# Performance work log

Measured on AMD Instinct MI355X. Metric: run time of the kernel, lower is better.

The kernel has to match this reference:

```python
import jax, jax.numpy as jnp
from jax import lax
import numpy as np

HEADS = 8

def _hswish(x):
    return x * jnp.clip(x + 3.0, 0.0, 6.0) / 6.0

def _sep_conv(x, dw, pw, pad):
    # depthwise conv (groups=C) followed by 1x1 pointwise conv, no bias
    dn = ('NCHW', 'OIHW', 'NCHW')
    y = lax.conv_general_dilated(x, dw, (1, 1), [(pad, pad), (pad, pad)],
                                 dimension_numbers=dn, feature_group_count=x.shape[1])
    return lax.conv_general_dilated(y, pw, (1, 1), [(0, 0), (0, 0)], dimension_numbers=dn)

def _bn(x, g, b, m, v):
    # SyncBatchNorm in eval mode (running stats), eps=1e-5
    inv = g / jnp.sqrt(v + 1e-5)
    return (x - m[:, None, None]) * inv[:, None, None] + b[:, None, None]

def _gn(x, g, b, groups=2):
    B, C, H, W = x.shape
    xg = x.reshape(B, groups, -1)
    mu = xg.mean(-1, keepdims=True)
    var = xg.var(-1, keepdims=True)
    xg = (xg - mu) / jnp.sqrt(var + 1e-5)
    return xg.reshape(B, C, H, W) * g[:, None, None] + b[:, None, None]

def _ln(x, g, b):
    mu = x.mean(-1, keepdims=True)
    var = x.var(-1, keepdims=True)
    return (x - mu) / jnp.sqrt(var + 1e-5) * g + b

def _forward(fl, h, w):
    (x, ln_q_g, ln_q_b, ln_k_g, ln_k_b, ln_v_g, ln_v_b, w_q, w_k, w_v, w_proj, b_proj,
     dw0, pw0, gn_g, gn_b, dw1, pw1, dw2, pw2,
     bn0_g, bn0_b, bn0_m, bn0_v, bn1_g, bn1_b, bn1_m, bn1_v, bn2_g, bn2_b, bn2_m, bn2_v) = fl
    B, C, N = x.shape  # C = attr_num tokens, N = dim = h*w
    d = N // HEADS
    scale = d ** -0.5
    q = _ln(x, ln_q_g, ln_q_b) @ w_q.T
    k = _ln(x, ln_k_g, ln_k_b) @ w_k.T
    v = _ln(x, ln_v_g, ln_v_b) @ w_v.T

    def agg(t):
        # aggregator(t.transpose(1,2), (h,w)) then head split; net input is (B,C,h,w)
        img = t.reshape(B, C, h, w)
        p0, p1, p2, p3 = jnp.split(img, 4, axis=1)  # seg_dim = C//4
        x0 = _hswish(_bn(p0, bn0_g, bn0_b, bn0_m, bn0_v))
        x1 = _hswish(_bn(_sep_conv(p1, dw1, pw1, 1), bn1_g, bn1_b, bn1_m, bn1_v))
        x2 = _hswish(_bn(_sep_conv(p2, dw2, pw2, 2), bn2_g, bn2_b, bn2_m, bn2_v))
        xl = _hswish(_gn(_sep_conv(p3, dw0, pw0, 1), gn_g, gn_b))
        y = jnp.concatenate([x0, x1, x2, xl], axis=1).reshape(B, C, N)
        return y.reshape(B, C, HEADS, d).transpose(0, 2, 1, 3)  # (B,H,C,d)

    qh, kh, vh = agg(q), agg(k), agg(v)
    scores = jnp.einsum('bhcd,bhkd->bhck', qh, kh)
    attn = jax.nn.softmax(jax.nn.gelu(scores, approximate=False) * scale, axis=-1)
    out = jnp.einsum('bhck,bhkd->bhcd', attn, vh).reshape(B, C, N)  # raw reshape as in torch
    out = out @ w_proj.T + b_proj
    out = out / jnp.maximum(jnp.linalg.norm(out, axis=-1, keepdims=True), 1e-12)
    return out, attn


def setup_inputs() -> dict:
    key = jax.random.key(0)
    ks = jax.random.split(key, 12)
    B, C, N = 32, 312, 1024
    sd = C // 4  # 78
    f32 = jnp.float32
    rn = lambda k, shp, s: jax.random.normal(k, shp, f32) * s
    inp = {
        'x': rn(ks[0], (B, C, N), 1.0),
        'h': 32, 'w': 32,
        'ln_q_g': jnp.ones((N,), f32), 'ln_q_b': jnp.zeros((N,), f32),
        'ln_k_g': jnp.ones((N,), f32), 'ln_k_b': jnp.zeros((N,), f32),
        'ln_v_g': jnp.ones((N,), f32), 'ln_v_b': jnp.zeros((N,), f32),
        'w_q': rn(ks[1], (N, N), N ** -0.5),
        'w_k': rn(ks[2], (N, N), N ** -0.5),
        'w_v': rn(ks[3], (N, N), N ** -0.5),
        'w_proj': rn(ks[4], (N, N), N ** -0.5),
        'b_proj': jnp.zeros((N,), f32),
        'dw0': rn(ks[5], (sd, 1, 3, 3), 1.0 / 3.0),
        'pw0': rn(ks[6], (sd, sd, 1, 1), sd ** -0.5),
        'gn_g': jnp.ones((sd,), f32), 'gn_b': jnp.zeros((sd,), f32),
        'dw1': rn(ks[7], (sd, 1, 3, 3), 1.0 / 3.0),
        'pw1': rn(ks[8], (sd, sd, 1, 1), sd ** -0.5),
        'dw2': rn(ks[9], (sd, 1, 5, 5), 1.0 / 5.0),
        'pw2': rn(ks[10], (sd, sd, 1, 1), sd ** -0.5),
    }
    for i in range(3):
        inp[f'bn{i}_g'] = jnp.ones((sd,), f32)
        inp[f'bn{i}_b'] = jnp.zeros((sd,), f32)
        inp[f'bn{i}_m'] = jnp.zeros((sd,), f32)
        inp[f'bn{i}_v'] = jnp.ones((sd,), f32)
    return inp


def reference(x, h, w, ln_q_g, ln_q_b, ln_k_g, ln_k_b, ln_v_g, ln_v_b, w_q, w_k, w_v, w_proj, b_proj, dw0, pw0, gn_g, gn_b, dw1, pw1, dw2, pw2, bn0_g, bn0_b, bn0_m, bn0_v, bn1_g, bn1_b, bn1_m, bn1_v, bn2_g, bn2_b, bn2_m, bn2_v):
    fl = (x, ln_q_g, ln_q_b, ln_k_g, ln_k_b, ln_v_g, ln_v_b, w_q, w_k, w_v, w_proj, b_proj,
          dw0, pw0, gn_g, gn_b, dw1, pw1, dw2, pw2,
          bn0_g, bn0_b, bn0_m, bn0_v, bn1_g, bn1_b, bn1_m, bn1_v, bn2_g, bn2_b, bn2_m, bn2_v)
    return _forward(fl, h, w)
```

## Files before the change

### kernel.cpp

```cpp
#include <hip/hip_runtime.h>
#include <hip/hip_bf16.h>
#include <float.h>

typedef __hip_bfloat16 bf16;
typedef __attribute__((ext_vector_type(8))) __bf16 bfrag;
typedef __attribute__((ext_vector_type(4))) float f32x4;

#define B_ 32
#define C_ 312
#define N_ 1024
#define H_ 8
#define D_ 128
#define SD_ 78
#define BC_ (B_ * C_)
#define BH_ (B_ * H_)

__device__ __forceinline__ float bf2f(bf16 x) { return __bfloat162float(x); }
__device__ __forceinline__ bf16 f2bf(float x) { return __float2bfloat16(x); }
__device__ __forceinline__ float hswish(float x) {
    return x * fminf(fmaxf(x + 3.0f, 0.0f), 6.0f) * (1.0f / 6.0f);
}

__device__ __forceinline__ void gload_lds16(const void* g, void* l) {
    __builtin_amdgcn_global_load_lds(
        (const __attribute__((address_space(1))) void*)g,
        (__attribute__((address_space(3))) void*)l, 16, 0, 0);
}

__global__ void ln_kernel(const float* __restrict__ x, bf16* __restrict__ xn) {
    int r = blockIdx.x;
    int t = threadIdx.x;
    const float* xr = x + (size_t)r * N_;
    float4 v4 = *reinterpret_cast<const float4*>(xr + t * 4);
    float s = v4.x + v4.y + v4.z + v4.w;
    float sq = v4.x * v4.x + v4.y * v4.y + v4.z * v4.z + v4.w * v4.w;
    __shared__ float rs[256], rq[256];
    rs[t] = s; rq[t] = sq; __syncthreads();
    for (int o = 128; o > 0; o >>= 1) {
        if (t < o) { rs[t] += rs[t + o]; rq[t] += rq[t + o]; }
        __syncthreads();
    }
    float mu = rs[0] * (1.0f / N_);
    float var = rq[0] * (1.0f / N_) - mu * mu;
    float rstd = rsqrtf(var + 1e-5f);
    __bf16 o4[4] = { (__bf16)((v4.x - mu) * rstd), (__bf16)((v4.y - mu) * rstd),
                     (__bf16)((v4.z - mu) * rstd), (__bf16)((v4.w - mu) * rstd) };
    *reinterpret_cast<uint2*>(reinterpret_cast<__bf16*>(xn) + (size_t)r * N_ + t * 4) =
        *reinterpret_cast<const uint2*>(o4);
}

__global__ void wcvt_kernel(const float* __restrict__ wq, const float* __restrict__ wk,
                            const float* __restrict__ wv, const float* __restrict__ wp,
                            const float* __restrict__ gq, const float* __restrict__ bq,
                            const float* __restrict__ gk, const float* __restrict__ bk,
                            const float* __restrict__ gv, const float* __restrict__ bv_,
                            bf16* __restrict__ wqkv, float* __restrict__ bias3,
                            bf16* __restrict__ wpb) {
    int n = blockIdx.x;
    int t = threadIdx.x;
    int k4 = t * 4;
    const float* src; const float* G = nullptr; const float* Bv = nullptr;
    if (n < 1024)      { src = wq + (size_t)n * N_;          G = gq; Bv = bq; }
    else if (n < 2048) { src = wk + (size_t)(n - 1024) * N_; G = gk; Bv = bk; }
    else if (n < 3072) { src = wv + (size_t)(n - 2048) * N_; G = gv; Bv = bv_; }
    else               { src = wp + (size_t)(n - 3072) * N_; }
    float4 w4 = *reinterpret_cast<const float4*>(src + k4);
    if (G) {
        __bf16 o[4] = { (__bf16)(w4.x * G[k4]),     (__bf16)(w4.y * G[k4 + 1]),
                        (__bf16)(w4.z * G[k4 + 2]), (__bf16)(w4.w * G[k4 + 3]) };
        *reinterpret_cast<uint2*>(wqkv + (size_t)n * N_ + k4) = *reinterpret_cast<const uint2*>(o);
        float s = w4.x * Bv[k4] + w4.y * Bv[k4 + 1] + w4.z * Bv[k4 + 2] + w4.w * Bv[k4 + 3];
        __shared__ float rs[256];
        rs[t] = s; __syncthreads();
        for (int o2 = 128; o2 > 0; o2 >>= 1) {
            if (t < o2) rs[t] += rs[t + o2];
            __syncthreads();
        }
        if (t == 0) bias3[n] = rs[0];
    } else {
        __bf16 o[4] = { (__bf16)w4.x, (__bf16)w4.y, (__bf16)w4.z, (__bf16)w4.w };
        *reinterpret_cast<uint2*>(wpb + (size_t)(n - 3072) * N_ + k4) = *reinterpret_cast<const uint2*>(o);
    }
}

template <bool OUTF32>
__global__ __launch_bounds__(256) void mfma_gemm_bw(
        const bf16* __restrict__ A_,
        const bf16* __restrict__ Wb,
        const float* __restrict__ bias, int nTx,
        void* __restrict__ O0, void* __restrict__ O1, void* __restrict__ O2) {
    const int K = 1024, Nout = 1024;
    __shared__ __bf16 sA[128 * 64];
    __shared__ __bf16 sB[128 * 64];
    const __bf16* A = reinterpret_cast<const __bf16*>(A_);
    const __bf16* W = reinterpret_cast<const __bf16*>(Wb);

    int t = threadIdx.x;
    int lane = t & 63, wave = t >> 6;
    int wm = (wave >> 1) * 64, wn = (wave & 1) * 64;
    int quad = lane >> 4, l15 = lane & 15;

    int cpx = gridDim.x >> 3;
    int tile = (blockIdx.x & 7) * cpx + (blockIdx.x >> 3);
    int bx = tile % nTx, by = tile / nTx;
    int m0 = by * 128;
    int w0 = bx * 128;
    int which = bx >> 3;
    int n0 = (bx & 7) * 128;

    int rowLoc = wave * 8 + (lane >> 3);
    int c8s = (lane & 7) ^ (lane >> 3);
    const __bf16* gA = A + (size_t)(m0 + rowLoc) * K + c8s * 8;
    const __bf16* gW = W + (size_t)(w0 + rowLoc) * K + c8s * 8;

    f32x4 acc[4][4];
#pragma unroll
    for (int i = 0; i < 4; i++)
#pragma unroll
        for (int j = 0; j < 4; j++) acc[i][j] = (f32x4)(0.f);

    for (int kt = 0; kt < 16; kt++) {
        int k0 = kt * 64;
#pragma unroll
        for (int cc = 0; cc < 4; cc++) {
            gload_lds16(gA + (size_t)cc * 32 * K + k0, &sA[cc * 2048 + wave * 512]);
            gload_lds16(gW + (size_t)cc * 32 * K + k0, &sB[cc * 2048 + wave * 512]);
        }
        __syncthreads();
#pragma unroll
        for (int kk = 0; kk < 2; kk++) {
            bfrag af[4], bfr[4];
#pragma unroll
            for (int mt = 0; mt < 4; mt++) {
                int row = wm + mt * 16 + l15;
                af[mt] = *reinterpret_cast<const bfrag*>(
                    &sA[(row * 8 + ((kk * 4 + quad) ^ (row & 7))) * 8]);
            }
#pragma unroll
            for (int nt = 0; nt < 4; nt++) {
                int row = wn + nt * 16 + l15;
                bfr[nt] = *reinterpret_cast<const bfrag*>(
                    &sB[(row * 8 + ((kk * 4 + quad) ^ (row & 7))) * 8]);
            }
#pragma unroll
            for (int mt = 0; mt < 4; mt++)
#pragma unroll
                for (int nt = 0; nt < 4; nt++)
                    acc[mt][nt] = __builtin_amdgcn_mfma_f32_16x16x32_bf16(af[mt], bfr[nt], acc[mt][nt], 0, 0, 0);
        }
        __syncthreads();
    }
    void* Cout = which == 0 ? O0 : (which == 1 ? O1 : O2);
#pragma unroll
    for (int mt = 0; mt < 4; mt++) {
#pragma unroll
        for (int nt = 0; nt < 4; nt++) {
            int cloc = wn + nt * 16 + l15;
            float bb = bias ? bias[w0 + cloc] : 0.f;
            int col = n0 + cloc;
#pragma unroll
            for (int r = 0; r < 4; r++) {
                int row = m0 + wm + mt * 16 + quad * 4 + r;
                float v = acc[mt][nt][r] + bb;
                if (OUTF32) ((float*)Cout)[(size_t)row * Nout + col] = v;
                else        ((bf16*)Cout)[(size_t)row * Nout + col] = f2bf(v);
            }
        }
    }
}

__global__ void seg0_kernel(const bf16* __restrict__ t0, const bf16* __restrict__ t1,
                            const bf16* __restrict__ t2,
                            bf16* __restrict__ h0, bf16* __restrict__ h1,
                            bf16* __restrict__ h2,
                            const float* __restrict__ g, const float* __restrict__ b,
                            const float* __restrict__ m, const float* __restrict__ v) {
    int ti = blockIdx.y;
    const bf16* tin = ti == 0 ? t0 : (ti == 1 ? t1 : t2);
    bf16* th = ti == 0 ? h0 : (ti == 1 ? h1 : h2);
    int bc = blockIdx.x;
    int bi = bc / SD_, c = bc % SD_;
    float inv = g[c] * rsqrtf(v[c] + 1e-5f);
    float mm = m[c], bb = b[c];
    const __bf16* tp = reinterpret_cast<const __bf16*>(tin) + ((size_t)bi * C_ + c) * N_;
    __bf16* base = reinterpret_cast<__bf16*>(th) + (size_t)bi * H_ * C_ * D_;
    int n = threadIdx.x * 4;
    uint2 in2 = *reinterpret_cast<const uint2*>(tp + n);
    const __bf16* iv = reinterpret_cast<const __bf16*>(&in2);
    __bf16 o4[4];
#pragma unroll
    for (int j = 0; j < 4; j++)
        o4[j] = (__bf16)hswish(((float)iv[j] - mm) * inv + bb);
    *reinterpret_cast<uint2*>(&base[((n >> 7) * C_ + c) * D_ + (n & 127)]) =
        *reinterpret_cast<const uint2*>(o4);
}

template <int KS, int MODE>
__device__ __forceinline__ void dwpw_impl(
        char* uMem, float* sWk, __bf16* dwT,
        const bf16* __restrict__ tin, int cOff,
        const float* __restrict__ dw, const float* __restrict__ pw,
        const float* __restrict__ g, const float* __restrict__ b,
        const float* __restrict__ m, const float* __restrict__ v,
        bf16* __restrict__ th, float* __restrict__ rawOut,
        int strip, int bi, int tid) {
    constexpr int WKP = ((KS * KS + 3) / 4) * 4;
    constexpr int NR  = KS + 1;
    __bf16* sIn = reinterpret_cast<__bf16*>(uMem);
    __bf16* sWm = reinterpret_cast<__bf16*>(uMem);
    const int P = KS / 2;

    for (int u = tid; u < SD_ * NR * 2; u += 512) {
        int rowi = u >> 1, side = u & 1;
        *reinterpret_cast<uint2*>(sIn + rowi * 40 + (side ? 36 : 0)) = make_uint2(0u, 0u);
    }
    for (int u = tid; u < 64 * 9; u += 512) {
        int pos = u / 9, cc = 78 + (u % 9) * 2;
        *reinterpret_cast<unsigned int*>(dwT + pos * 96 + cc) = 0u;
    }
    const __bf16* tbase = reinterpret_cast<const __bf16*>(tin) + ((size_t)bi * C_ + cOff) * N_;
    for (int u = tid; u < SD_ * NR * 4; u += 512) {
        int c = u / (NR * 4);
        int rem = u - c * (NR * 4);
        int di = rem >> 2, cb = rem & 3;
        int ii = 2 * strip + di - P;
        uint4 val = make_uint4(0u, 0u, 0u, 0u);
        if (ii >= 0 && ii <= 31)
            val = *reinterpret_cast<const uint4*>(tbase + (size_t)c * N_ + ii * 32 + cb * 8);
        __bf16* dst = sIn + (c * NR + di) * 40 + 4 + cb * 8;
        *reinterpret_cast<uint2*>(dst)     = make_uint2(val.x, val.y);
        *reinterpret_cast<uint2*>(dst + 4) = make_uint2(val.z, val.w);
    }
    for (int i = tid; i < SD_ * KS * KS; i += 512) {
        int c = i / (KS * KS), q = i - c * (KS * KS);
        sWk[c * WKP + q] = dw[i];
    }
    __syncthreads();

    for (int u = tid; u < SD_ * 8; u += 512) {
        int c = u >> 3, grp = u & 7;
        int row = grp >> 2, q8 = (grp & 3) << 3;
        const __bf16* rbase = sIn + (size_t)(c * NR + row) * 40;
        __bf16 rowv[KS][16];
#pragma unroll
        for (int di = 0; di < KS; di++) {
            *reinterpret_cast<bfrag*>(&rowv[di][0]) = *reinterpret_cast<const bfrag*>(rbase + di * 40 + q8);
            *reinterpret_cast<bfrag*>(&rowv[di][8]) = *reinterpret_cast<const bfrag*>(rbase + di * 40 + q8 + 8);
        }
        float wreg[WKP];
#pragma unroll
        for (int qq = 0; qq < WKP / 4; qq++)
            *reinterpret_cast<float4*>(&wreg[qq * 4]) =
                *reinterpret_cast<const float4*>(&sWk[c * WKP + qq * 4]);
        float acc8[8];
#pragma unroll
        for (int k = 0; k < 8; k++) acc8[k] = 0.f;
#pragma unroll
        for (int di = 0; di < KS; di++) {
#pragma unroll
            for (int dj = 0; dj < KS; dj++) {
                float w = wreg[di * KS + dj];
#pragma unroll
                for (int k = 0; k < 8; k++)
                    acc8[k] += (float)rowv[di][k + dj - P + 4] * w;
            }
        }
#pragma unroll
        for (int k = 0; k < 8; k++)
            dwT[(row * 32 + q8 + k) * 96 + c] = (__bf16)acc8[k];
    }
    __syncthreads();

    for (int u = tid; u < 80 * 96; u += 512) {
        int o = u / 96, c = u - o * 96;
        float val = (o < SD_ && c < SD_) ? pw[o * SD_ + c] : 0.f;
        sWm[u] = (__bf16)val;
    }
    __syncthreads();

    int lane = tid & 63, wave = tid >> 6;
    int quad = lane >> 4, l15 = lane & 15;
    int wn = wave & 3, mh = wave >> 2;
    int mt0 = mh ? 3 : 0;
    int mcnt = mh ? 2 : 3;
    f32x4 acc[3];
#pragma unroll
    for (int i = 0; i < 3; i++) acc[i] = (f32x4)(0.f);
#pragma unroll
    for (int kk = 0; kk < 3; kk++) {
        bfrag bv = *reinterpret_cast<const bfrag*>(dwT + (wn * 16 + l15) * 96 + kk * 32 + quad * 8);
#pragma unroll
        for (int mi = 0; mi < 3; mi++) {
            if (mi < mcnt) {
                bfrag av = *reinterpret_cast<const bfrag*>(sWm + ((mt0 + mi) * 16 + l15) * 96 + kk * 32 + quad * 8);
                acc[mi] = __builtin_amdgcn_mfma_f32_16x16x32_bf16(av, bv, acc[mi], 0, 0, 0);
            }
        }
    }
    int n = strip * 64 + wn * 16 + l15;
    if (MODE == 0) {
        bf16* base = th + (size_t)bi * H_ * C_ * D_;
#pragma unroll
        for (int mi = 0; mi < 3; mi++) {
            if (mi < mcnt) {
#pragma unroll
                for (int r = 0; r < 4; r++) {
                    int o = (mt0 + mi) * 16 + quad * 4 + r;
                    if (o < SD_) {
                        float inv = g[o] * rsqrtf(v[o] + 1e-5f);
                        float y = hswish((acc[mi][r] - m[o]) * inv + b[o]);
                        base[((n >> 7) * C_ + cOff + o) * D_ + (n & 127)] = f2bf(y);
                    }
                }
            }
        }
    } else {
        float* opr = rawOut + (size_t)bi * SD_ * N_;
#pragma unroll
        for (int mi = 0; mi < 3; mi++) {
            if (mi < mcnt) {
#pragma unroll
                for (int r = 0; r < 4; r++) {
                    int o = (mt0 + mi) * 16 + quad * 4 + r;
                    if (o < SD_) opr[(size_t)o * N_ + n] = acc[mi][r];
                }
            }
        }
    }
}

__global__ __launch_bounds__(512) void dwpw_all_kernel(
        const bf16* __restrict__ t0, const bf16* __restrict__ t1,
        const bf16* __restrict__ t2,
        const float* __restrict__ dw1, const float* __restrict__ pw1,
        const float* __restrict__ g1, const float* __restrict__ b1,
        const float* __restrict__ m1, const float* __restrict__ v1,
        const float* __restrict__ dw2, const float* __restrict__ pw2,
        const float* __restrict__ g2, const float* __restrict__ b2,
        const float* __restrict__ m2, const float* __restrict__ v2,
        const float* __restrict__ dw0, const float* __restrict__ pw0,
        bf16* __restrict__ h0, bf16* __restrict__ h1, bf16* __restrict__ h2,
        float* __restrict__ r0_, float* __restrict__ r1_, float* __restrict__ r2_) {
    __shared__ __align__(16) char uMem[SD_ * 6 * 40 * sizeof(__bf16)];
    __shared__ __align__(16) float sWk[SD_ * 28];
    __shared__ __align__(16) __bf16 dwT[64 * 96];

    int ti = blockIdx.y;
    const bf16* tin = ti == 0 ? t0 : (ti == 1 ? t1 : t2);
    bf16* th = ti == 0 ? h0 : (ti == 1 ? h1 : h2);
    float* rawOut = ti == 0 ? r0_ : (ti == 1 ? r1_ : r2_);
    int strip = blockIdx.x & 15;
    int bi = blockIdx.x >> 4;
    int tid = threadIdx.x;
    int branch = blockIdx.z;

    if (branch == 0) {
        dwpw_impl<3, 0>(uMem, sWk, dwT, tin, SD_, dw1, pw1, g1, b1, m1, v1,
                        th, (float*)nullptr, strip, bi, tid);
    } else if (branch == 1) {
        dwpw_impl<5, 0>(uMem, sWk, dwT, tin, 2 * SD_, dw2, pw2, g2, b2, m2, v2,
                        th, (float*)nullptr, strip, bi, tid);
    } else {
        dwpw_impl<3, 1>(uMem, sWk, dwT, tin, 3 * SD_, dw0, pw0,
                        (const float*)nullptr, (const float*)nullptr,
                        (const float*)nullptr, (const float*)nullptr,
                        (bf16*)nullptr, rawOut, strip, bi, tid);
    }
}

__global__ void gn_stats_kernel(const float* __restrict__ r0_, const float* __restrict__ r1_,
                                const float* __restrict__ r2_, float* __restrict__ stats) {
    int ti = blockIdx.y;
    const float* tmp2 = ti == 0 ? r0_ : (ti == 1 ? r1_ : r2_);
    int bg = blockIdx.x;
    int bi = bg >> 1, grp = bg & 1;
    const float* p = tmp2 + (size_t)bi * SD_ * N_ + (size_t)grp * 39 * N_;
    float s = 0.f, sq = 0.f;
    const int TOT = 39 * N_;
    for (int i = threadIdx.x * 4; i < TOT; i += 1024) {
        float4 f4 = *reinterpret_cast<const float4*>(p + i);
        s += f4.x + f4.y + f4.z + f4.w;
        sq += f4.x * f4.x + f4.y * f4.y + f4.z * f4.z + f4.w * f4.w;
    }
    __shared__ float rs[256], rq[256];
    rs[threadIdx.x] = s; rq[threadIdx.x] = sq; __syncthreads();
    for (int o = 128; o > 0; o >>= 1) {
        if (threadIdx.x < o) { rs[threadIdx.x] += rs[threadIdx.x + o]; rq[threadIdx.x] += rq[threadIdx.x + o]; }
        __syncthreads();
    }
    if (threadIdx.x == 0) {
        float mu = rs[0] / (float)TOT;
        float var = rq[0] / (float)TOT - mu * mu;
        stats[ti * 128 + bg * 2] = mu;
        stats[ti * 128 + bg * 2 + 1] = rsqrtf(var + 1e-5f);
    }
}

__global__ void gn_apply_kernel(const float* __restrict__ r0_, const float* __restrict__ r1_,
                                const float* __restrict__ r2_, const float* __restrict__ stats,
                                const float* __restrict__ gg, const float* __restrict__ gb,
                                bf16* __restrict__ h0, bf16* __restrict__ h1,
                                bf16* __restrict__ h2) {
    int ti = blockIdx.y;
    const float* tmp2 = ti == 0 ? r0_ : (ti == 1 ? r1_ : r2_);
    bf16* th = ti == 0 ? h0 : (ti == 1 ? h1 : h2);
    int bc = blockIdx.x;
    int bi = bc / SD_, c = bc % SD_;
    int grp = c / 39;
    float mu = stats[ti * 128 + (bi * 2 + grp) * 2];
    float rstd = stats[ti * 128 + (bi * 2 + grp) * 2 + 1];
    float sc = gg[c] * rstd;
    float of = gb[c] - mu * sc;
    const float* p = tmp2 + ((size_t)bi * SD_ + c) * N_;
    __bf16* base = reinterpret_cast<__bf16*>(th) + (size_t)bi * H_ * C_ * D_;
    int n = threadIdx.x * 4;
    float4 f4 = *reinterpret_cast<const float4*>(p + n);
    __bf16 o4[4] = { (__bf16)hswish(f4.x * sc + of), (__bf16)hswish(f4.y * sc + of),
                     (__bf16)hswish(f4.z * sc + of), (__bf16)hswish(f4.w * sc + of) };
    *reinterpret_cast<uint2*>(&base[((n >> 7) * C_ + 234 + c) * D_ + (n & 127)]) =
        *reinterpret_cast<const uint2*>(o4);
}

#define SLDA 136
#define PLDA 328
__global__ __launch_bounds__(512, 4) void attn_av_kernel(
        const bf16* __restrict__ qh_, const bf16* __restrict__ kh_,
        const bf16* __restrict__ vh_,
        float* __restrict__ attnOut, bf16* __restrict__ ctx) {
    __shared__ __align__(16) char uni[60928];
    __shared__ float smax[64][2];
    __shared__ float ssum[64][2];
    __bf16* sQ = reinterpret_cast<__bf16*>(uni);
    __bf16* sK = reinterpret_cast<__bf16*>(uni + 17408);
    __bf16* sP = reinterpret_cast<__bf16*>(uni);
    __bf16* sV = reinterpret_cast<__bf16*>(uni + 41984);
    const __bf16* qh = reinterpret_cast<const __bf16*>(qh_);
    const __bf16* kh = reinterpret_cast<const __bf16*>(kh_);
    const __bf16* vh = reinterpret_cast<const __bf16*>(vh_);

    int strip = blockIdx.x;
    int bh = blockIdx.y;
    int t = threadIdx.x;
    int lane = t & 63, wave = t >> 6;
    int quad = lane >> 4, l15 = lane & 15;
    int wm = wave >> 1;
    int wn = wave & 1;

#pragma unroll
    for (int cc = 0; cc < 2; cc++) {
        int c = t + cc * 512;
        int row = c >> 4, seg = c & 15;
        int src = strip * 64 + row; if (src > 311) src = 311;
        bfrag v = *reinterpret_cast<const bfrag*>(qh + ((size_t)bh * C_ + src) * D_ + seg * 8);
        *reinterpret_cast<bfrag*>(&sQ[row * SLDA + seg * 8]) = v;
    }

    f32x4 acc[10];
#pragma unroll
    for (int i = 0; i < 10; i++) acc[i] = (f32x4)(0.f);

    bfrag af[4];
    bool afLoaded = false;

    for (int half = 0; half < 2; half++) {
        if (half) __syncthreads();
        for (int cc = 0; cc < 5; cc++) {
            int c = t + cc * 512;
            int row = c >> 4, seg = c & 15;
            int src = half * 160 + row;
            bfrag v;
            if (src < C_) {
                v = *reinterpret_cast<const bfrag*>(kh + ((size_t)bh * C_ + src) * D_ + seg * 8);
            } else {
#pragma unroll
                for (int j = 0; j < 8; j++) v[j] = (__bf16)0.f;
            }
            *reinterpret_cast<bfrag*>(&sK[row * SLDA + seg * 8]) = v;
        }
        __syncthreads();
        if (!afLoaded) {
#pragma unroll
            for (int ks = 0; ks < 4; ks++)
                af[ks] = *reinterpret_cast<const bfrag*>(&sQ[(wm * 16 + l15) * SLDA + ks * 32 + quad * 8]);
            afLoaded = true;
        }
#pragma unroll
        for (int ks = 0; ks < 4; ks++) {
#pragma unroll
            for (int jj = 0; jj < 5; jj++) {
                int lr = (wn * 5 + jj) * 16 + l15;
                bfrag bf = *reinterpret_cast<const bfrag*>(&sK[lr * SLDA + ks * 32 + quad * 8]);
                acc[half * 5 + jj] = __builtin_amdgcn_mfma_f32_16x16x32_bf16(af[ks], bf, acc[half * 5 + jj], 0, 0, 0);
            }
        }
    }

    const float scale = 0.08838834764831845f;
    const float inv_sqrt2 = 0.7071067811865475f;
#pragma unroll
    for (int a = 0; a < 10; a++) {
        int gt = (a / 5) * 10 + wn * 5 + (a % 5);
        int col = gt * 16 + l15;
#pragma unroll
        for (int r = 0; r < 4; r++) {
            float v = acc[a][r];
            float ge = 0.5f * v * (1.0f + erff(v * inv_sqrt2));
            float s = ge * scale;
            if (col >= C_) s = -FLT_MAX;
            acc[a][r] = s;
        }
    }
    float mx[4];
#pragma unroll
    for (int r = 0; r < 4; r++) {
        float m = -FLT_MAX;
#pragma unroll
        for (int a = 0; a < 10; a++) m = fmaxf(m, acc[a][r]);
        for (int o = 1; o < 16; o <<= 1) m = fmaxf(m, __shfl_xor(m, o));
        mx[r] = m;
    }
    if (l15 == 0) {
#pragma unroll
        for (int r = 0; r < 4; r++) smax[wm * 16 + quad * 4 + r][wn] = mx[r];
    }
    __syncthreads();
    float sm[4];
#pragma unroll
    for (int r = 0; r < 4; r++) {
        int row = wm * 16 + quad * 4 + r;
        float m = fmaxf(smax[row][0], smax[row][1]);
        float s = 0.f;
#pragma unroll
        for (int a = 0; a < 10; a++) {
            float e = __expf(acc[a][r] - m);
            acc[a][r] = e;
            s += e;
        }
        for (int o = 1; o < 16; o <<= 1) s += __shfl_xor(s, o);
        sm[r] = s;
    }
    if (l15 == 0) {
#pragma unroll
        for (int r = 0; r < 4; r++) ssum[wm * 16 + quad * 4 + r][wn] = sm[r];
    }
    __syncthreads();

#pragma unroll
    for (int r = 0; r < 4; r++) {
        int row = wm * 16 + quad * 4 + r;
        float inv = 1.0f / (ssum[row][0] + ssum[row][1]);
        int grow = strip * 64 + row;
        float* ao = attnOut + ((size_t)bh * C_ + grow) * C_;
#pragma unroll
        for (int a = 0; a < 10; a++) {
            int gt = (a / 5) * 10 + wn * 5 + (a % 5);
            int col = gt * 16 + l15;
            float pv = acc[a][r] * inv;
            if (grow < C_ && col < C_) ao[col] = pv;
            sP[row * PLDA + col] = f2bf(pv);
        }
    }

    f32x4 acc2[4];
#pragma unroll
    for (int i = 0; i < 4; i++) acc2[i] = (f32x4)(0.f);

    auto stageV = [&](int chunk) {
#pragma unroll
        for (int it = 0; it < 2; it++) {
            int g = t + it * 512;
            int d = g & 127;
            int oct = g >> 7;
            int ktl = oct >> 2, quad2 = oct & 3;
            int cb = chunk * 64 + ktl * 32 + quad2 * 8;
            const __bf16* vp = vh + ((size_t)bh * C_ + cb) * D_ + d;
            bfrag v;
            if (cb + 7 < C_) {
#pragma unroll
                for (int j = 0; j < 8; j++) v[j] = vp[(size_t)j * D_];
            } else {
#pragma unroll
                for (int j = 0; j < 8; j++) v[j] = (cb + j < C_) ? vp[(size_t)j * D_] : (__bf16)0.f;
            }
            *reinterpret_cast<bfrag*>(&sV[(((ktl * 8 + (d >> 4)) * 64) + quad2 * 16 + (d & 15)) * 8]) = v;
        }
    };

    stageV(0);
    __syncthreads();

    for (int chunk = 0; chunk < 5; chunk++) {
#pragma unroll
        for (int ktl = 0; ktl < 2; ktl++) {
            bfrag a = *reinterpret_cast<const bfrag*>(
                &sP[(wm * 16 + l15) * PLDA + chunk * 64 + ktl * 32 + quad * 8]);
#pragma unroll
            for (int ntl = 0; ntl < 4; ntl++) {
                int ntg = wn * 4 + ntl;
                bfrag b = *reinterpret_cast<const bfrag*>(&sV[(((ktl * 8 + ntg) * 64) + lane) * 8]);
                acc2[ntl] = __builtin_amdgcn_mfma_f32_16x16x32_bf16(a, b, acc2[ntl], 0, 0, 0);
            }
        }
        if (chunk < 4) {
            __syncthreads();
            stageV(chunk + 1);
            __syncthreads();
        }
    }

    int b = bh >> 3, h = bh & 7;
#pragma unroll
    for (int ntl = 0; ntl < 4; ntl++) {
        int d = wn * 64 + ntl * 16 + l15;
#pragma unroll
        for (int r = 0; r < 4; r++) {
            int c = strip * 64 + wm * 16 + quad * 4 + r;
            if (c < C_) {
                size_t oi = ((size_t)b * C_ + h * 39 + (c >> 3)) * N_ + ((c & 7) << 7) + d;
                ctx[oi] = f2bf(acc2[ntl][r]);
            }
        }
    }
}

__global__ void norm_kernel(const float* __restrict__ out3, float* __restrict__ outp) {
    int r = blockIdx.x;
    const float* p = out3 + (size_t)r * N_;
    float4 f4 = *reinterpret_cast<const float4*>(p + threadIdx.x * 4);
    float sq = f4.x * f4.x + f4.y * f4.y + f4.z * f4.z + f4.w * f4.w;
    __shared__ float rq[256];
    rq[threadIdx.x] = sq; __syncthreads();
    for (int o = 128; o > 0; o >>= 1) {
        if (threadIdx.x < o) rq[threadIdx.x] += rq[threadIdx.x + o];
        __syncthreads();
    }
    float inv = 1.0f / fmaxf(sqrtf(rq[0]), 1e-12f);
    float4 o4 = { f4.x * inv, f4.y * inv, f4.z * inv, f4.w * inv };
    *reinterpret_cast<float4*>(outp + (size_t)r * N_ + threadIdx.x * 4) = o4;
}

extern "C" void kernel_launch(void* const* d_in, const int* in_sizes, int n_in,
                              void* d_out, int out_size, void* d_ws, size_t ws_size,
                              hipStream_t stream) {
    const float* x      = (const float*)d_in[0];
    const float* ln_q_g = (const float*)d_in[3];
    const float* ln_q_b = (const float*)d_in[4];
    const float* ln_k_g = (const float*)d_in[5];
    const float* ln_k_b = (const float*)d_in[6];
    const float* ln_v_g = (const float*)d_in[7];
    const float* ln_v_b = (const float*)d_in[8];
    const float* w_q    = (const float*)d_in[9];
    const float* w_k    = (const float*)d_in[10];
    const float* w_v    = (const float*)d_in[11];
    const float* w_proj = (const float*)d_in[12];
    const float* b_proj = (const float*)d_in[13];
    const float* dw0    = (const float*)d_in[14];
    const float* pw0    = (const float*)d_in[15];
    const float* gn_g   = (const float*)d_in[16];
    const float* gn_b   = (const float*)d_in[17];
    const float* dw1    = (const float*)d_in[18];
    const float* pw1    = (const float*)d_in[19];
    const float* dw2    = (const float*)d_in[20];
    const float* pw2    = (const float*)d_in[21];
    const float* bn0_g  = (const float*)d_in[22];
    const float* bn0_b  = (const float*)d_in[23];
    const float* bn0_m  = (const float*)d_in[24];
    const float* bn0_v  = (const float*)d_in[25];
    const float* bn1_g  = (const float*)d_in[26];
    const float* bn1_b  = (const float*)d_in[27];
    const float* bn1_m  = (const float*)d_in[28];
    const float* bn1_v  = (const float*)d_in[29];
    const float* bn2_g  = (const float*)d_in[30];
    const float* bn2_b  = (const float*)d_in[31];
    const float* bn2_m  = (const float*)d_in[32];
    const float* bn2_v  = (const float*)d_in[33];

    char* ws = (char*)d_ws;
    size_t off = 0;
    auto alloc = [&](size_t bytes) {
        void* p = ws + off;
        off = (off + bytes + 255) & ~(size_t)255;
        return p;
    };
    const size_t BF_BYTES = (size_t)BC_ * N_ * sizeof(bf16);
    const size_t T2_FLOATS = (size_t)B_ * SD_ * N_;
    bf16*  xn   = (bf16*)alloc(BF_BYTES);
    bf16*  qb   = (bf16*)alloc(BF_BYTES);
    bf16*  kb   = (bf16*)alloc(BF_BYTES);
    bf16*  vb   = (bf16*)alloc(BF_BYTES);
    float* tmp2 = (float*)alloc(3 * T2_FLOATS * sizeof(float));
    float* gnst = (float*)alloc(2048);
    bf16*  wqkv = (bf16*)alloc((size_t)3 * N_ * N_ * sizeof(bf16));
    float* bias3 = (float*)alloc((size_t)3 * N_ * sizeof(float));
    bf16*  wpb  = (bf16*)alloc((size_t)N_ * N_ * sizeof(bf16));

    float* out_main = (float*)d_out;
    float* attn_out = out_main + (size_t)BC_ * N_;

    bf16* qh  = xn;
    bf16* kh  = (bf16*)out_main;
    bf16* vh  = kh + (size_t)BC_ * N_;
    bf16* ctx = vb;
    float* out3 = (float*)qb;
    float* r0 = tmp2, *r1 = tmp2 + T2_FLOATS, *r2 = tmp2 + 2 * T2_FLOATS;

    hipLaunchKernelGGL(wcvt_kernel, dim3(4096), dim3(256), 0, stream,
                       w_q, w_k, w_v, w_proj,
                       ln_q_g, ln_q_b, ln_k_g, ln_k_b, ln_v_g, ln_v_b,
                       wqkv, bias3, wpb);
    hipLaunchKernelGGL(ln_kernel, dim3(BC_), dim3(256), 0, stream, x, xn);
    hipLaunchKernelGGL((mfma_gemm_bw<false>), dim3(24 * 78), dim3(256), 0, stream,
                       xn, wqkv, bias3, 24, (void*)qb, (void*)kb, (void*)vb);

    hipLaunchKernelGGL(seg0_kernel, dim3(B_ * SD_, 3), dim3(256), 0, stream,
                       qb, kb, vb, qh, kh, vh, bn0_g, bn0_b, bn0_m, bn0_v);
    hipLaunchKernelGGL(dwpw_all_kernel, dim3(B_ * 16, 3, 3), dim3(512), 0, stream,
                       qb, kb, vb,
                       dw1, pw1, bn1_g, bn1_b, bn1_m, bn1_v,
                       dw2, pw2, bn2_g, bn2_b, bn2_m, bn2_v,
                       dw0, pw0,
                       qh, kh, vh, r0, r1, r2);
    hipLaunchKernelGGL(gn_stats_kernel, dim3(B_ * 2, 3), dim3(256), 0, stream,
                       r0, r1, r2, gnst);
    hipLaunchKernelGGL(gn_apply_kernel, dim3(B_ * SD_, 3), dim3(256), 0, stream,
                       r0, r1, r2, gnst, gn_g, gn_b, qh, kh, vh);

    hipLaunchKernelGGL(attn_av_kernel, dim3(5, BH_), dim3(512), 0, stream,
                       qh, kh, vh, attn_out, ctx);
    hipLaunchKernelGGL((mfma_gemm_bw<true>), dim3(8 * 78), dim3(256), 0, stream,
                       ctx, wpb, b_proj, 8, (void*)out3, (void*)out3, (void*)out3);
    hipLaunchKernelGGL(norm_kernel, dim3(BC_), dim3(256), 0, stream, out3, out_main);
}
```

Baseline: 560.6 us.

## Fold seg0 BN-hswish into dwpw kernel and swizzle dwT LDS layout

Removes the standalone seg0 kernel and runs its BN plus hswish work as a fourth z-branch of the dwpw_all kernel, saving one launch. The transposed depthwise buffer is widened to a 128-element row with an XOR swizzle on 8-element chunks, and the pointwise weight tile gets a 104-element row pitch. Both layout changes aim to cut LDS bank conflicts on the MFMA fragment loads. In exchange, dwT now needs more LDS and a full zero-fill, and the extra branch blocks still reserve the kernel's large static LDS, which may lower occupancy.

```diff
diff --git a/kernel.cpp b/kernel.cpp
--- a/kernel.cpp
+++ b/kernel.cpp
@@ -25,6 +25,10 @@
     __builtin_amdgcn_global_load_lds(
         (const __attribute__((address_space(1))) void*)g,
         (__attribute__((address_space(3))) void*)l, 16, 0, 0);
+}
+
+__device__ __forceinline__ int dwt_idx(int pos, int c) {
+    return pos * 128 + ((((c >> 3) ^ (pos & 7) ^ ((pos >> 3) & 7)) * 8) | (c & 7));
 }
 
 __global__ void ln_kernel(const float* __restrict__ x, bf16* __restrict__ xn) {
@@ -169,32 +173,6 @@
     }
 }
 
-__global__ void seg0_kernel(const bf16* __restrict__ t0, const bf16* __restrict__ t1,
-                            const bf16* __restrict__ t2,
-                            bf16* __restrict__ h0, bf16* __restrict__ h1,
-                            bf16* __restrict__ h2,
-                            const float* __restrict__ g, const float* __restrict__ b,
-                            const float* __restrict__ m, const float* __restrict__ v) {
-    int ti = blockIdx.y;
-    const bf16* tin = ti == 0 ? t0 : (ti == 1 ? t1 : t2);
-    bf16* th = ti == 0 ? h0 : (ti == 1 ? h1 : h2);
-    int bc = blockIdx.x;
-    int bi = bc / SD_, c = bc % SD_;
-    float inv = g[c] * rsqrtf(v[c] + 1e-5f);
-    float mm = m[c], bb = b[c];
-    const __bf16* tp = reinterpret_cast<const __bf16*>(tin) + ((size_t)bi * C_ + c) * N_;
-    __bf16* base = reinterpret_cast<__bf16*>(th) + (size_t)bi * H_ * C_ * D_;
-    int n = threadIdx.x * 4;
-    uint2 in2 = *reinterpret_cast<const uint2*>(tp + n);
-    const __bf16* iv = reinterpret_cast<const __bf16*>(&in2);
-    __bf16 o4[4];
-#pragma unroll
-    for (int j = 0; j < 4; j++)
-        o4[j] = (__bf16)hswish(((float)iv[j] - mm) * inv + bb);
-    *reinterpret_cast<uint2*>(&base[((n >> 7) * C_ + c) * D_ + (n & 127)]) =
-        *reinterpret_cast<const uint2*>(o4);
-}
-
 template <int KS, int MODE>
 __device__ __forceinline__ void dwpw_impl(
         char* uMem, float* sWk, __bf16* dwT,
@@ -214,9 +192,8 @@
         int rowi = u >> 1, side = u & 1;
         *reinterpret_cast<uint2*>(sIn + rowi * 40 + (side ? 36 : 0)) = make_uint2(0u, 0u);
     }
-    for (int u = tid; u < 64 * 9; u += 512) {
-        int pos = u / 9, cc = 78 + (u % 9) * 2;
-        *reinterpret_cast<unsigned int*>(dwT + pos * 96 + cc) = 0u;
+    for (int u = tid; u < 64 * 128 / 8; u += 512) {
+        *reinterpret_cast<uint4*>(dwT + u * 8) = make_uint4(0u, 0u, 0u, 0u);
     }
     const __bf16* tbase = reinterpret_cast<const __bf16*>(tin) + ((size_t)bi * C_ + cOff) * N_;
     for (int u = tid; u < SD_ * NR * 4; u += 512) {
@@ -267,12 +244,12 @@
         }
 #pragma unroll
         for (int k = 0; k < 8; k++)
-            dwT[(row * 32 + q8 + k) * 96 + c] = (__bf16)acc8[k];
+            dwT[dwt_idx(row * 32 + q8 + k, c)] = (__bf16)acc8[k];
     }
     __syncthreads();
 
-    for (int u = tid; u < 80 * 96; u += 512) {
-        int o = u / 96, c = u - o * 96;
+    for (int u = tid; u < 80 * 104; u += 512) {
+        int o = u / 104, c = u - o * 104;
         float val = (o < SD_ && c < SD_) ? pw[o * SD_ + c] : 0.f;
         sWm[u] = (__bf16)val;
     }
@@ -288,11 +265,13 @@
     for (int i = 0; i < 3; i++) acc[i] = (f32x4)(0.f);
 #pragma unroll
     for (int kk = 0; kk < 3; kk++) {
-        bfrag bv = *reinterpret_cast<const bfrag*>(dwT + (wn * 16 + l15) * 96 + kk * 32 + quad * 8);
+        int prow = wn * 16 + l15;
+        int ch = (kk * 4 + quad) ^ (prow & 7) ^ ((prow >> 3) & 7);
+        bfrag bv = *reinterpret_cast<const bfrag*>(dwT + prow * 128 + ch * 8);
 #pragma unroll
         for (int mi = 0; mi < 3; mi++) {
             if (mi < mcnt) {
-                bfrag av = *reinterpret_cast<const bfrag*>(sWm + ((mt0 + mi) * 16 + l15) * 96 + kk * 32 + quad * 8);
+                bfrag av = *reinterpret_cast<const bfrag*>(sWm + ((mt0 + mi) * 16 + l15) * 104 + kk * 32 + quad * 8);
                 acc[mi] = __builtin_amdgcn_mfma_f32_16x16x32_bf16(av, bv, acc[mi], 0, 0, 0);
             }
         }
@@ -339,11 +318,13 @@
         const float* __restrict__ g2, const float* __restrict__ b2,
         const float* __restrict__ m2, const float* __restrict__ v2,
         const float* __restrict__ dw0, const float* __restrict__ pw0,
+        const float* __restrict__ g0, const float* __restrict__ b0,
+        const float* __restrict__ m0, const float* __restrict__ v0,
         bf16* __restrict__ h0, bf16* __restrict__ h1, bf16* __restrict__ h2,
         float* __restrict__ r0_, float* __restrict__ r1_, float* __restrict__ r2_) {
     __shared__ __align__(16) char uMem[SD_ * 6 * 40 * sizeof(__bf16)];
     __shared__ __align__(16) float sWk[SD_ * 28];
-    __shared__ __align__(16) __bf16 dwT[64 * 96];
+    __shared__ __align__(16) __bf16 dwT[64 * 128];
 
     int ti = blockIdx.y;
     const bf16* tin = ti == 0 ? t0 : (ti == 1 ? t1 : t2);
@@ -353,6 +334,26 @@
     int bi = blockIdx.x >> 4;
     int tid = threadIdx.x;
     int branch = blockIdx.z;
+
+    if (branch == 3) {
+        const __bf16* tb = reinterpret_cast<const __bf16*>(tin) + (size_t)bi * C_ * N_;
+        __bf16* base = reinterpret_cast<__bf16*>(th) + (size_t)bi * H_ * C_ * D_;
+        for (int u = tid; u < SD_ * 16; u += 512) {
+            int c = u >> 4, p4 = u & 15;
+            int n = strip * 64 + p4 * 4;
+            uint2 in2 = *reinterpret_cast<const uint2*>(tb + (size_t)c * N_ + n);
+            const __bf16* iv = reinterpret_cast<const __bf16*>(&in2);
+            float inv = g0[c] * rsqrtf(v0[c] + 1e-5f);
+            float mm = m0[c], bb = b0[c];
+            __bf16 o4[4];
+#pragma unroll
+            for (int j = 0; j < 4; j++)
+                o4[j] = (__bf16)hswish(((float)iv[j] - mm) * inv + bb);
+            *reinterpret_cast<uint2*>(&base[((n >> 7) * C_ + c) * D_ + (n & 127)]) =
+                *reinterpret_cast<const uint2*>(o4);
+        }
+        return;
+    }
 
     if (branch == 0) {
         dwpw_impl<3, 0>(uMem, sWk, dwT, tin, SD_, dw1, pw1, g1, b1, m1, v1,
@@ -712,13 +713,11 @@
     hipLaunchKernelGGL((mfma_gemm_bw<false>), dim3(24 * 78), dim3(256), 0, stream,
                        xn, wqkv, bias3, 24, (void*)qb, (void*)kb, (void*)vb);
 
-    hipLaunchKernelGGL(seg0_kernel, dim3(B_ * SD_, 3), dim3(256), 0, stream,
-                       qb, kb, vb, qh, kh, vh, bn0_g, bn0_b, bn0_m, bn0_v);
-    hipLaunchKernelGGL(dwpw_all_kernel, dim3(B_ * 16, 3, 3), dim3(512), 0, stream,
+    hipLaunchKernelGGL(dwpw_all_kernel, dim3(B_ * 16, 3, 4), dim3(512), 0, stream,
                        qb, kb, vb,
                        dw1, pw1, bn1_g, bn1_b, bn1_m, bn1_v,
                        dw2, pw2, bn2_g, bn2_b, bn2_m, bn2_v,
-                       dw0, pw0,
+                       dw0, pw0, bn0_g, bn0_b, bn0_m, bn0_v,
                        qh, kh, vh, r0, r1, r2);
     hipLaunchKernelGGL(gn_stats_kernel, dim3(B_ * 2, 3), dim3(256), 0, stream,
                        r0, r1, r2, gnst);
```

Measured after the change: 548.0 us. 1.02x faster.
